# Performance work log

Measured on AMD Instinct MI355X. Metric: run time of the kernel, lower is better.

## Reference

```python
import jax, jax.numpy as jnp
import numpy as np

DIM = 256
N_PATCHES = 2048
N_HEADS = 8
BATCH = 2


def setup_inputs() -> dict:
    key = jax.random.key(0)
    ks = jax.random.split(key, 8)
    d = DIM
    s = d ** -0.5
    return {
        "x": jax.random.normal(ks[0], (BATCH, N_PATCHES, d), dtype=jnp.float32),
        # weights stored (in_features, out_features) so y = x @ W + b
        "W_qk": jax.random.normal(ks[1], (d, 2 * d), dtype=jnp.float32) * s,
        "W_v": jax.random.normal(ks[2], (d, d), dtype=jnp.float32) * s,
        "W_proj": jax.random.normal(ks[3], (d, d), dtype=jnp.float32) * s,
        "b_proj": jnp.zeros((d,), dtype=jnp.float32),
        "W_pos": jax.random.normal(ks[4], (2, N_HEADS), dtype=jnp.float32) * 0.5,
        "b_pos": jnp.zeros((N_HEADS,), dtype=jnp.float32),
        "gating": jnp.ones((N_HEADS,), dtype=jnp.float32),
    }


def reference(x, W_qk, W_v, W_proj, b_proj, W_pos, b_pos, gating):
    B, N, C = x.shape
    H = gating.shape[0]
    Dh = C // H
    scale = Dh ** -0.5

    # content attention: q @ k^T softmax
    qk = (x @ W_qk).reshape(B, N, 2, H, Dh)
    q = jnp.transpose(qk[:, :, 0], (0, 2, 1, 3))  # [B,H,N,Dh]
    k = jnp.transpose(qk[:, :, 1], (0, 2, 1, 3))
    patch_score = jax.nn.softmax(jnp.einsum("bhnd,bhmd->bhnm", q, k) * scale, axis=-1)

    # positional attention from relative indices (d, |d|) -> per-head score
    idx = jnp.arange(N, dtype=jnp.float32)
    rel = idx[:, None] - idx[None, :]                      # [N,N]
    rel_feat = jnp.stack([rel, jnp.abs(rel)], axis=-1)     # [N,N,2]
    pos = rel_feat @ W_pos + b_pos                         # [N,N,H]
    pos_score = jax.nn.softmax(jnp.transpose(pos, (2, 0, 1)), axis=-1)  # [H,N,N]

    g = jax.nn.sigmoid(gating)[None, :, None, None]        # [1,H,1,1]
    attn = (1.0 - g) * patch_score + g * pos_score[None]   # [B,H,N,N]
    attn = attn / jnp.sum(attn, axis=-1, keepdims=True)

    v = jnp.transpose((x @ W_v).reshape(B, N, H, Dh), (0, 2, 1, 3))  # [B,H,N,Dh]
    out = jnp.einsum("bhnm,bhmd->bhnd", attn, v)
    out = jnp.transpose(out, (0, 2, 1, 3)).reshape(B, N, C)
    return out @ W_proj + b_proj
```

## Files before the change

### kernel.cpp

```cpp
#include <hip/hip_runtime.h>
#include <hip/hip_bf16.h>
#include <hip/hip_fp16.h>

#define DIM 256
#define NP 2048
#define NH 8
#define BATCH 2
#define DH 32

typedef __attribute__((ext_vector_type(8))) short bshort8;
typedef __attribute__((ext_vector_type(4))) short bshort4;
typedef __attribute__((ext_vector_type(4))) float f32x4;

#define LOG2E 1.44269504f
#define QSCALE (0.17677669529663687f * LOG2E)

union U16B { uint4 u; bshort8 s8; bshort4 s4x[2]; __hip_bfloat16 h[8]; };
union U8B  { uint2 u; bshort4 s4; __hip_bfloat16 h[4]; };

__device__ __forceinline__ float fexp2(float x) { return __builtin_amdgcn_exp2f(x); }
__device__ __forceinline__ unsigned packbf(float hi, float lo) {
    return __builtin_amdgcn_perm(__float_as_uint(hi), __float_as_uint(lo), 0x07060302u);
}
__device__ __forceinline__ void gl16(const void* g, void* l) {
    __builtin_amdgcn_global_load_lds(
        (const __attribute__((address_space(1))) void*)g,
        (__attribute__((address_space(3))) void*)l, 16, 0, 0);
}
__device__ __forceinline__ int lds_addr(int row, int colg) {
    return row * 256 + (((colg ^ (row & 7)) & 31) << 3);
}

__global__ __launch_bounds__(256) void prep_kernel(
    const float* __restrict__ Wqk,
    const float* __restrict__ Wv,
    const float* __restrict__ Wproj,
    const float* __restrict__ x,
    __hip_bfloat16* __restrict__ WT,
    __hip_bfloat16* __restrict__ xb) {
    const int t = threadIdx.x;
    const int blk = blockIdx.x;
    if (blk >= 64) {
        const int base = (blk - 64) * 256 + t;
#pragma unroll
        for (int i = 0; i < 16; i++) {
            const int idx = base + i * 16384;
            float4 f = *(const float4*)(x + (size_t)idx * 4);
            U8B a;
            a.h[0] = __float2bfloat16(f.x); a.h[1] = __float2bfloat16(f.y);
            a.h[2] = __float2bfloat16(f.z); a.h[3] = __float2bfloat16(f.w);
            *(uint2*)(xb + (size_t)idx * 4) = a.u;
        }
        return;
    }
    __shared__ float ts[64][65];
    const int ct = blk >> 2, k0 = (blk & 3) * 64;
    const int c0 = ct * 64;
    const float* src; int ldw, cs0; float scl = 1.0f;
    if (ct < 8)       { src = Wqk;   ldw = 512; cs0 = c0;      if (ct < 4) scl = QSCALE; }
    else if (ct < 12) { src = Wv;    ldw = 256; cs0 = c0 - 512; }
    else              { src = Wproj; ldw = 256; cs0 = c0 - 768; }
    const int cc = t & 63, tq = t >> 6;
#pragma unroll
    for (int j = 0; j < 16; j++) {
        int kk = tq * 16 + j;
        ts[kk][cc] = src[(size_t)(k0 + kk) * ldw + cs0 + cc];
    }
    __syncthreads();
    const int kk2 = t & 63;
#pragma unroll
    for (int j = 0; j < 16; j++) {
        int cc2 = tq * 16 + j;
        WT[(size_t)(c0 + cc2) * 256 + k0 + kk2] = __float2bfloat16(ts[kk2][cc2] * scl);
    }
}

__global__ __launch_bounds__(256) void qkv_mfma(
    const __hip_bfloat16* __restrict__ xb,
    const __hip_bfloat16* __restrict__ WT,
    __hip_bfloat16* __restrict__ qT,
    __hip_bfloat16* __restrict__ k,
    __hip_bfloat16* __restrict__ vT) {
    __shared__ __align__(16) __hip_bfloat16 As[64 * 256];
    __shared__ __align__(16) __hip_bfloat16 Bs[64 * 256];
    const int t = threadIdx.x, lane = t & 63, wvid = t >> 6;
    const int l15 = lane & 15, l4 = lane >> 4;
    const int m0 = blockIdx.x * 64;
    const int nb0 = blockIdx.y * 64;
    const int nc = nb0 + wvid * 16 + l15;
    const int lrow = lane >> 5, lcg = lane & 31;

#pragma unroll
    for (int j = 0; j < 8; j++) {
        const int r0 = j * 8 + wvid * 2;
        const int row = r0 + lrow;
        const int cgs = (lcg ^ (row & 7)) & 31;
        gl16(xb + (((size_t)(m0 + row)) << 8) + cgs * 8, (char*)As + r0 * 512);
        gl16(WT + (((size_t)(nb0 + row)) << 8) + cgs * 8, (char*)Bs + r0 * 512);
    }
    __syncthreads();

    f32x4 acc[4] = {{0.f,0.f,0.f,0.f},{0.f,0.f,0.f,0.f},{0.f,0.f,0.f,0.f},{0.f,0.f,0.f,0.f}};
#pragma unroll
    for (int kk = 0; kk < 8; kk++) {
        const int colg = kk * 4 + l4;
        U16B bw; bw.u = *(const uint4*)&Bs[lds_addr(wvid * 16 + l15, colg)];
#pragma unroll
        for (int mt = 0; mt < 4; mt++) {
            U16B ax; ax.u = *(const uint4*)&As[lds_addr(mt * 16 + l15, colg)];
            acc[mt] = __builtin_amdgcn_mfma_f32_16x16x32_bf16(ax.s8, bw.s8, acc[mt], 0, 0, 0);
        }
    }

    if (nb0 < 256) {
        const int b = m0 >> 11;
#pragma unroll
        for (int mt = 0; mt < 4; mt++) {
            int tokn = (m0 & (NP - 1)) + mt * 16 + l4 * 4;
            U8B vv;
#pragma unroll
            for (int r = 0; r < 4; r++) vv.h[r] = __float2bfloat16(acc[mt][r]);
            *(uint2*)(qT + (size_t)(b * 256 + nc) * NP + tokn) = vv.u;
        }
    } else if (nb0 < 512) {
        const int c = nc - 256, h = c >> 5, d = c & 31;
#pragma unroll
        for (int mt = 0; mt < 4; mt++)
#pragma unroll
            for (int r = 0; r < 4; r++) {
                int tok = m0 + mt * 16 + l4 * 4 + r;
                int b = tok >> 11, n = tok & (NP - 1);
                k[((size_t)(b * NH + h) * NP + n) * DH + d] = __float2bfloat16(acc[mt][r]);
            }
    } else {
        const int c = nc - 512;
        const int b = m0 >> 11;
#pragma unroll
        for (int mt = 0; mt < 4; mt++) {
            int tokn = (m0 & (NP - 1)) + mt * 16 + l4 * 4;
            U8B vv;
#pragma unroll
            for (int r = 0; r < 4; r++) vv.h[r] = __float2bfloat16(acc[mt][r]);
            *(uint2*)(vT + (size_t)(b * 256 + c) * NP + tokn) = vv.u;
        }
    }
}

__global__ __launch_bounds__(512) void pos_scan(
    const __hip_bfloat16* __restrict__ vTg,
    const float* __restrict__ Wpos,
    __half* __restrict__ NF,
    __half* __restrict__ NB,
    float* __restrict__ lpF,
    float* __restrict__ lpB) {
    __shared__ float Lc[40][8];
    __shared__ float Cin[40][8];
    const int t = threadIdx.x;
    const int bh = blockIdx.x >> 1, dir = blockIdx.x & 1;
    const int h = bh & (NH - 1), b = bh >> 3;
    const float w0 = Wpos[h] * LOG2E, w1 = Wpos[NH + h] * LOG2E;
    const float rate = dir ? (w1 - w0) : (w0 + w1);
    const float mr = fexp2(fminf(rate, 0.f));
    const float mrate = fmaxf(rate, 0.f);
    const bool isV = (t < 256);
    const bool isD = (t >= 256 && t < 264);
    const bool act = isV || isD;
    const int ch  = isV ? (t & 31) : 32;
    const int seg = isV ? (t >> 5) : (t - 256);
    const int n0 = dir ? (seg * 256 + 255) : (seg * 256);
    const int stp = dir ? -1 : 1;
    const float dist0 = dir ? (float)(2047 - n0) : (float)n0;
    const float scl0 = fexp2(-mrate * dist0);
    float sdp[8];
#pragma unroll
    for (int j = 0; j < 8; j++) sdp[j] = fexp2(-mrate * (float)j);
    const float sd8 = fexp2(-mrate * 8.f);
    const __hip_bfloat16* vrow = vTg + ((size_t)(b * 256 + h * 32 + (ch & 31))) * NP;

    if (act) {
        float F = 0.f, sclc = scl0;
        int n = n0;
#pragma unroll 4
        for (int c = 0; c < 32; ++c) {
            float Wv[8];
            if (isV) {
                U16B vv; vv.u = *(const uint4*)(vrow + (dir ? n - 7 : n));
#pragma unroll
                for (int j = 0; j < 8; j++)
                    Wv[j] = sdp[j] * __bfloat162float(vv.h[dir ? 7 - j : j]);
            } else {
#pragma unroll
                for (int j = 0; j < 8; j++) Wv[j] = sdp[j];
            }
#pragma unroll
            for (int j = 0; j < 8; j++) F = fmaf(mr, F, sclc * Wv[j]);
            sclc *= sd8;
            n += 8 * stp;
        }
        Lc[ch][seg] = F;
    }
    __syncthreads();
    if (t < 33) {
        const float A = fexp2(fminf(rate, 0.f) * 256.f);
        float C = 0.f;
        for (int s = 0; s < 8; ++s) {
            const int ss = dir ? (7 - s) : s;
            Cin[t][ss] = C;
            C = fmaf(A, C, Lc[t][ss]);
        }
    }
    __syncthreads();
    if (act) {
        float Fc = Cin[ch][seg], sclc = scl0;
        int n = n0;
        __half* nout = dir ? NB : NF;
        float* lout = dir ? lpB : lpF;
#pragma unroll 4
        for (int c = 0; c < 32; ++c) {
            if (isV) {
                U16B vv; vv.u = *(const uint4*)(vrow + (dir ? n - 7 : n));
#pragma unroll
                for (int j = 0; j < 8; j++) {
                    float tt = sclc * (sdp[j] * __bfloat162float(vv.h[dir ? 7 - j : j]));
                    Fc = fmaf(mr, Fc, tt);
                    float outv = dir ? (Fc - tt) : Fc;
                    nout[((size_t)bh * NP + n + j * stp) * 32 + ch] = __float2half(outv);
                }
            } else {
#pragma unroll
                for (int j = 0; j < 8; j++) {
                    float tt = sclc * sdp[j];
                    Fc = fmaf(mr, Fc, tt);
                    float outv = dir ? (Fc - tt) : Fc;
                    lout[(size_t)bh * NP + n + j * stp] = outv;
                }
            }
            sclc *= sd8;
            n += 8 * stp;
        }
    }
}

__global__ __launch_bounds__(512, 4) void attn_kernel(
    const __hip_bfloat16* __restrict__ qg,
    const __hip_bfloat16* __restrict__ kg,
    const __hip_bfloat16* __restrict__ vTg,
    const float* __restrict__ Wpos,
    const float* __restrict__ gating,
    const __half* __restrict__ NF,
    const __half* __restrict__ NB,
    const float* __restrict__ lpF,
    const float* __restrict__ lpB,
    __hip_bfloat16* __restrict__ ao) {
    __shared__ __align__(16) __hip_bfloat16 Kt[2][2][64][40];
    __shared__ __align__(16) __hip_bfloat16 Vt[2][2][32][72];
    __shared__ float cmb[4][32][16];
    __shared__ float cls[4][16];

    const int t = threadIdx.x;
    const int lane = t & 63, wvid = t >> 6;
    const int l15 = lane & 15, l4 = lane >> 4;
    const int qt = wvid & 3, kh = wvid >> 2;
    const int bh = blockIdx.x >> 5, qb = blockIdx.x & 31;
    const int h = bh & (NH - 1), b = bh >> 3;
    const int q0 = qb * 64 + qt * 16;
    const int myq = q0 + l15;

    const int st_ = t & 255;
    const int kstart = kh * 1024;
    const __hip_bfloat16* kptr = kg + (size_t)bh * NP * DH + (size_t)(kstart + (st_ >> 2)) * DH + (st_ & 3) * 8;
    const __hip_bfloat16* vptr = vTg + ((size_t)bh * DH + (st_ >> 3)) * NP + kstart + (st_ & 7) * 8;

    const int vd = st_ >> 3, vs = st_ & 7;
    const int vc0 = ((2 * vs) & 3) * 16 + (vs >> 1) * 4;
    const int vc1 = ((2 * vs + 1) & 3) * 16 + (vs >> 1) * 4;

    uint4 kreg = *(const uint4*)kptr;
    uint4 vreg = *(const uint4*)vptr;
    *(uint4*)&Kt[kh][0][st_ >> 2][(st_ & 3) * 8] = kreg;
    *(uint2*)&Vt[kh][0][vd][vc0] = make_uint2(vreg.x, vreg.y);
    *(uint2*)&Vt[kh][0][vd][vc1] = make_uint2(vreg.z, vreg.w);

    const float w0 = Wpos[h] * LOG2E;
    const float w1 = Wpos[NH + h] * LOG2E;
    const float g = 1.0f / (1.0f + __expf(-gating[h]));
    const float nf = (float)myq;

    U16B qv;
#pragma unroll
    for (int j = 0; j < 8; j++)
        qv.h[j] = qg[((size_t)bh * DH + l4 * 8 + j) * NP + myq];

    __syncthreads();

    f32x4 os0 = {0.f,0.f,0.f,0.f}, os1 = {0.f,0.f,0.f,0.f};
    float ls = 0.f;

    for (int it = 0; it < 16; ++it) {
        const int cur = it & 1, nxt = cur ^ 1;

        if (it < 15) {
            kreg = *(const uint4*)(kptr + (size_t)(it + 1) * 64 * DH);
            vreg = *(const uint4*)(vptr + (it + 1) * 64);
        }

        f32x4 st4[4];
#pragma unroll
        for (int kt = 0; kt < 4; kt++) {
            U16B kf; kf.u = *(const uint4*)&Kt[kh][cur][kt * 16 + l15][l4 * 8];
            st4[kt] = __builtin_amdgcn_mfma_f32_16x16x32_bf16(
                kf.s8, qv.s8, (f32x4){0.f,0.f,0.f,0.f}, 0, 0, 0);
        }

        U16B va0, va1, vb0, vb1;
        {
            const __hip_bfloat16* v0 = &Vt[kh][cur][l15][l4 * 16];
            const __hip_bfloat16* v1 = &Vt[kh][cur][16 + l15][l4 * 16];
            va0.u = *(const uint4*)v0;
            va1.u = *(const uint4*)(v0 + 8);
            vb0.u = *(const uint4*)v1;
            vb1.u = *(const uint4*)(v1 + 8);
        }

#pragma unroll
        for (int kt = 0; kt < 4; kt++) {
            const bshort4 fa = (kt < 2) ? va0.s4x[kt & 1] : va1.s4x[kt & 1];
            const bshort4 fb = (kt < 2) ? vb0.s4x[kt & 1] : vb1.s4x[kt & 1];
            float es0 = fexp2(st4[kt][0]), es1 = fexp2(st4[kt][1]);
            float es2 = fexp2(st4[kt][2]), es3 = fexp2(st4[kt][3]);
            ls += (es0 + es1) + (es2 + es3);
            U8B pc;
            pc.u.x = packbf(es1, es0); pc.u.y = packbf(es3, es2);
            os0 = __builtin_amdgcn_mfma_f32_16x16x16bf16_1k(fa, pc.s4, os0, 0, 0, 0);
            os1 = __builtin_amdgcn_mfma_f32_16x16x16bf16_1k(fb, pc.s4, os1, 0, 0, 0);
        }

        if (it < 15) {
            *(uint4*)&Kt[kh][nxt][st_ >> 2][(st_ & 3) * 8] = kreg;
            *(uint2*)&Vt[kh][nxt][vd][vc0] = make_uint2(vreg.x, vreg.y);
            *(uint2*)&Vt[kh][nxt][vd][vc1] = make_uint2(vreg.z, vreg.w);
        }
        __syncthreads();
    }

    ls += __shfl_xor(ls, 16, 64); ls += __shfl_xor(ls, 32, 64);

    if (kh == 1) {
#pragma unroll
        for (int r = 0; r < 4; r++) {
            cmb[qt][l4 * 4 + r][l15]      = os0[r];
            cmb[qt][16 + l4 * 4 + r][l15] = os1[r];
        }
        if (l4 == 0) cls[qt][l15] = ls;
    }
    __syncthreads();
    if (kh == 0) {
        ls += cls[qt][l15];
        const float cs = (1.0f - g) / ls;
        const float pmF = fmaxf(0.f, (w0 + w1) * nf);
        const float pmB = fmaxf(0.f, (w1 - w0) * (2047.f - nf));
        const float pm  = fmaxf(pmF, pmB);
        const float eF = fexp2(pmF - pm);
        const float eB = fexp2(pmB - pm);
        const size_t lpi = (size_t)bh * NP + myq;
        const float lpv = eF * lpF[lpi] + eB * lpB[lpi];
        const float cp = g / lpv;
        const __half* nfp = NF + lpi * 32 + l4 * 4;
        const __half* nbp = NB + lpi * 32 + l4 * 4;
        const size_t orow = ((size_t)b * NP + myq) * DIM + h * DH;
        U8B o0, o1;
#pragma unroll
        for (int r = 0; r < 4; r++) {
            float p0 = eF * __half2float(nfp[r])      + eB * __half2float(nbp[r]);
            float p1 = eF * __half2float(nfp[16 + r]) + eB * __half2float(nbp[16 + r]);
            o0.h[r] = __float2bfloat16(cs * (os0[r] + cmb[qt][l4 * 4 + r][l15]) + cp * p0);
            o1.h[r] = __float2bfloat16(cs * (os1[r] + cmb[qt][16 + l4 * 4 + r][l15]) + cp * p1);
        }
        *(uint2*)(ao + orow + l4 * 4)      = o0.u;
        *(uint2*)(ao + orow + 16 + l4 * 4) = o1.u;
    }
}

__global__ __launch_bounds__(256) void proj_mfma(
    const __hip_bfloat16* __restrict__ ao,
    const __hip_bfloat16* __restrict__ WT,
    const float* __restrict__ bias,
    float* __restrict__ out) {
    __shared__ __align__(16) __hip_bfloat16 As[64 * 256];
    __shared__ __align__(16) __hip_bfloat16 Bs[64 * 256];
    const int t = threadIdx.x, lane = t & 63, wvid = t >> 6;
    const int l15 = lane & 15, l4 = lane >> 4;
    const int m0 = blockIdx.x * 64;
    const int nb0 = blockIdx.y * 64;
    const int nc = nb0 + wvid * 16 + l15;
    const int lrow = lane >> 5, lcg = lane & 31;

#pragma unroll
    for (int j = 0; j < 8; j++) {
        const int r0 = j * 8 + wvid * 2;
        const int row = r0 + lrow;
        const int cgs = (lcg ^ (row & 7)) & 31;
        gl16(ao + (((size_t)(m0 + row)) << 8) + cgs * 8, (char*)As + r0 * 512);
        gl16(WT + (((size_t)(768 + nb0 + row)) << 8) + cgs * 8, (char*)Bs + r0 * 512);
    }
    __syncthreads();

    f32x4 acc[4] = {{0.f,0.f,0.f,0.f},{0.f,0.f,0.f,0.f},{0.f,0.f,0.f,0.f},{0.f,0.f,0.f,0.f}};
#pragma unroll
    for (int kk = 0; kk < 8; kk++) {
        const int colg = kk * 4 + l4;
        U16B bw; bw.u = *(const uint4*)&Bs[lds_addr(wvid * 16 + l15, colg)];
#pragma unroll
        for (int mt = 0; mt < 4; mt++) {
            U16B ax; ax.u = *(const uint4*)&As[lds_addr(mt * 16 + l15, colg)];
            acc[mt] = __builtin_amdgcn_mfma_f32_16x16x32_bf16(ax.s8, bw.s8, acc[mt], 0, 0, 0);
        }
    }

    const float bb = bias[nc];
#pragma unroll
    for (int mt = 0; mt < 4; mt++)
#pragma unroll
        for (int r = 0; r < 4; r++) {
            int tok = m0 + mt * 16 + l4 * 4 + r;
            out[(size_t)tok * 256 + nc] = acc[mt][r] + bb;
        }
}

extern "C" void kernel_launch(void* const* d_in, const int* in_sizes, int n_in,
                              void* d_out, int out_size, void* d_ws, size_t ws_size,
                              hipStream_t stream) {
    const float* x      = (const float*)d_in[0];
    const float* Wqk    = (const float*)d_in[1];
    const float* Wv     = (const float*)d_in[2];
    const float* Wproj  = (const float*)d_in[3];
    const float* bproj  = (const float*)d_in[4];
    const float* Wpos   = (const float*)d_in[5];
    const float* gating = (const float*)d_in[7];
    float* out = (float*)d_out;

    char* w = (char*)d_ws;
    __hip_bfloat16* WT = (__hip_bfloat16*)w;
    __hip_bfloat16* qT = WT + 262144;
    __hip_bfloat16* k  = qT + 1048576;
    __hip_bfloat16* vT = k  + 1048576;
    __hip_bfloat16* ao = vT + 1048576;
    __hip_bfloat16* xb = ao + 1048576;
    __half* NF = (__half*)(w + 11010048);
    __half* NB = (__half*)(w + 13107200);
    float* lpF = (float*)(w + 15204352);
    float* lpB = (float*)(w + 15335424);

    prep_kernel<<<128, 256, 0, stream>>>(Wqk, Wv, Wproj, x, WT, xb);
    qkv_mfma<<<dim3(64, 12), 256, 0, stream>>>(xb, WT, qT, k, vT);
    pos_scan<<<32, 512, 0, stream>>>(vT, Wpos, NF, NB, lpF, lpB);
    attn_kernel<<<BATCH * NH * (NP / 64), 512, 0, stream>>>(qT, k, vT, Wpos, gating,
                                                            NF, NB, lpF, lpB, ao);
    proj_mfma<<<dim3(64, 4), 256, 0, stream>>>(ao, WT, bproj, out);
}
```

Before: 123.1 us.

## Fuse positional scan into attention kernel with semaphore; compute normalizers analytically

```diff
diff --git a/kernel.cpp b/kernel.cpp
--- a/kernel.cpp
+++ b/kernel.cpp
@@ -13,6 +13,7 @@
 typedef __attribute__((ext_vector_type(4))) float f32x4;
 
 #define LOG2E 1.44269504f
+#define LN2F 0.6931472f
 #define QSCALE (0.17677669529663687f * LOG2E)
 
 union U16B { uint4 u; bshort8 s8; bshort4 s4x[2]; __hip_bfloat16 h[8]; };
@@ -146,122 +147,103 @@
     }
 }
 
-__global__ __launch_bounds__(512) void pos_scan(
-    const __hip_bfloat16* __restrict__ vTg,
-    const float* __restrict__ Wpos,
-    __half* __restrict__ NF,
-    __half* __restrict__ NB,
-    float* __restrict__ lpF,
-    float* __restrict__ lpB) {
-    __shared__ float Lc[40][8];
-    __shared__ float Cin[40][8];
-    const int t = threadIdx.x;
-    const int bh = blockIdx.x >> 1, dir = blockIdx.x & 1;
-    const int h = bh & (NH - 1), b = bh >> 3;
-    const float w0 = Wpos[h] * LOG2E, w1 = Wpos[NH + h] * LOG2E;
-    const float rate = dir ? (w1 - w0) : (w0 + w1);
-    const float mr = fexp2(fminf(rate, 0.f));
-    const float mrate = fmaxf(rate, 0.f);
-    const bool isV = (t < 256);
-    const bool isD = (t >= 256 && t < 264);
-    const bool act = isV || isD;
-    const int ch  = isV ? (t & 31) : 32;
-    const int seg = isV ? (t >> 5) : (t - 256);
-    const int n0 = dir ? (seg * 256 + 255) : (seg * 256);
-    const int stp = dir ? -1 : 1;
-    const float dist0 = dir ? (float)(2047 - n0) : (float)n0;
-    const float scl0 = fexp2(-mrate * dist0);
-    float sdp[8];
-#pragma unroll
-    for (int j = 0; j < 8; j++) sdp[j] = fexp2(-mrate * (float)j);
-    const float sd8 = fexp2(-mrate * 8.f);
-    const __hip_bfloat16* vrow = vTg + ((size_t)(b * 256 + h * 32 + (ch & 31))) * NP;
-
-    if (act) {
-        float F = 0.f, sclc = scl0;
-        int n = n0;
-#pragma unroll 4
-        for (int c = 0; c < 32; ++c) {
-            float Wv[8];
-            if (isV) {
-                U16B vv; vv.u = *(const uint4*)(vrow + (dir ? n - 7 : n));
-#pragma unroll
-                for (int j = 0; j < 8; j++)
-                    Wv[j] = sdp[j] * __bfloat162float(vv.h[dir ? 7 - j : j]);
-            } else {
-#pragma unroll
-                for (int j = 0; j < 8; j++) Wv[j] = sdp[j];
-            }
-#pragma unroll
-            for (int j = 0; j < 8; j++) F = fmaf(mr, F, sclc * Wv[j]);
-            sclc *= sd8;
-            n += 8 * stp;
-        }
-        Lc[ch][seg] = F;
-    }
-    __syncthreads();
-    if (t < 33) {
-        const float A = fexp2(fminf(rate, 0.f) * 256.f);
-        float C = 0.f;
-        for (int s = 0; s < 8; ++s) {
-            const int ss = dir ? (7 - s) : s;
-            Cin[t][ss] = C;
-            C = fmaf(A, C, Lc[t][ss]);
-        }
-    }
-    __syncthreads();
-    if (act) {
-        float Fc = Cin[ch][seg], sclc = scl0;
-        int n = n0;
-        __half* nout = dir ? NB : NF;
-        float* lout = dir ? lpB : lpF;
-#pragma unroll 4
-        for (int c = 0; c < 32; ++c) {
-            if (isV) {
-                U16B vv; vv.u = *(const uint4*)(vrow + (dir ? n - 7 : n));
-#pragma unroll
-                for (int j = 0; j < 8; j++) {
-                    float tt = sclc * (sdp[j] * __bfloat162float(vv.h[dir ? 7 - j : j]));
-                    Fc = fmaf(mr, Fc, tt);
-                    float outv = dir ? (Fc - tt) : Fc;
-                    nout[((size_t)bh * NP + n + j * stp) * 32 + ch] = __float2half(outv);
-                }
-            } else {
-#pragma unroll
-                for (int j = 0; j < 8; j++) {
-                    float tt = sclc * sdp[j];
-                    Fc = fmaf(mr, Fc, tt);
-                    float outv = dir ? (Fc - tt) : Fc;
-                    lout[(size_t)bh * NP + n + j * stp] = outv;
-                }
-            }
-            sclc *= sd8;
-            n += 8 * stp;
-        }
-    }
-}
-
 __global__ __launch_bounds__(512, 4) void attn_kernel(
     const __hip_bfloat16* __restrict__ qg,
     const __hip_bfloat16* __restrict__ kg,
     const __hip_bfloat16* __restrict__ vTg,
     const float* __restrict__ Wpos,
     const float* __restrict__ gating,
-    const __half* __restrict__ NF,
-    const __half* __restrict__ NB,
-    const float* __restrict__ lpF,
-    const float* __restrict__ lpB,
-    __hip_bfloat16* __restrict__ ao) {
+    __half* __restrict__ NF,
+    __half* __restrict__ NB,
+    __hip_bfloat16* __restrict__ ao,
+    unsigned* __restrict__ sem) {
     __shared__ __align__(16) __hip_bfloat16 Kt[2][2][64][40];
     __shared__ __align__(16) __hip_bfloat16 Vt[2][2][32][72];
     __shared__ float cmb[4][32][16];
     __shared__ float cls[4][16];
 
     const int t = threadIdx.x;
+    const int bid = blockIdx.x;
+
+    if (bid < 64) {
+        float* scanL = &cmb[0][0][0];
+        float* scanC = scanL + 544;
+        const int sbh = bid >> 2, dir = (bid >> 1) & 1, cg = bid & 1;
+        const int sh = sbh & (NH - 1), sb = sbh >> 3;
+        const int seg = t >> 4, ch16 = t & 15, sch = cg * 16 + ch16;
+        const float sw0 = Wpos[sh] * LOG2E, sw1 = Wpos[NH + sh] * LOG2E;
+        const float rate = dir ? (sw1 - sw0) : (sw0 + sw1);
+        const float mr = fexp2(fminf(rate, 0.f));
+        const float mrate = fmaxf(rate, 0.f);
+        const int n0 = seg * 64;
+        const float dist0 = dir ? (float)(1984 - n0) : (float)n0;
+        float sclc = fexp2(-mrate * dist0);
+        const float sd8 = fexp2(-mrate * 8.f);
+        float sdp[8], mrp[9];
+#pragma unroll
+        for (int j = 0; j < 8; j++) sdp[j] = fexp2(-mrate * (float)j);
+        mrp[0] = 1.f;
+#pragma unroll
+        for (int j = 1; j < 9; j++) mrp[j] = mrp[j - 1] * mr;
+        const float mr8 = mrp[8];
+        const __hip_bfloat16* vrow = vTg + ((size_t)(sb * 256 + sh * 32 + sch)) * NP;
+
+        float S[64];
+        float F = 0.f;
+#pragma unroll
+        for (int c = 0; c < 8; c++) {
+            U16B vv;
+            vv.u = *(const uint4*)(vrow + (dir ? (n0 + 56 - c * 8) : (n0 + c * 8)));
+#pragma unroll
+            for (int j = 0; j < 8; j++) {
+                float V = __bfloat162float(vv.h[dir ? 7 - j : j]);
+                float inp = sclc * (sdp[j] * V);
+                float Fp = F;
+                F = fmaf(mr, F, inp);
+                S[c * 8 + j] = dir ? (mr * Fp) : F;
+            }
+            sclc *= sd8;
+        }
+        scanL[ch16 * 33 + seg] = F;
+        __syncthreads();
+        if (t < 16) {
+            const float A64 = fexp2(fminf(rate, 0.f) * 64.f);
+            float C = 0.f;
+            for (int idx = 0; idx < 32; ++idx) {
+                const int s = dir ? (31 - idx) : idx;
+                scanC[t * 33 + s] = C;
+                C = fmaf(A64, C, scanL[t * 33 + s]);
+            }
+        }
+        __syncthreads();
+        {
+            const float Cin = scanC[ch16 * 33 + seg];
+            __half* nout = dir ? NB : NF;
+            float cm = Cin;
+#pragma unroll
+            for (int c = 0; c < 8; c++) {
+#pragma unroll
+                for (int j = 0; j < 8; j++) {
+                    const int i = c * 8 + j;
+                    float outv = fmaf(cm, mrp[j + 1], S[i]);
+                    const int ni = dir ? (n0 + 63 - i) : (n0 + i);
+                    nout[((size_t)sbh * NP + ni) * 32 + sch] = __float2half(outv);
+                }
+                cm *= mr8;
+            }
+        }
+        __syncthreads();
+        if (t == 0) {
+            __threadfence();
+            __hip_atomic_fetch_add(sem, 1u, __ATOMIC_RELEASE, __HIP_MEMORY_SCOPE_AGENT);
+        }
+        __syncthreads();
+    }
+
     const int lane = t & 63, wvid = t >> 6;
     const int l15 = lane & 15, l4 = lane >> 4;
     const int qt = wvid & 3, kh = wvid >> 2;
-    const int bh = blockIdx.x >> 5, qb = blockIdx.x & 31;
+    const int bh = bid >> 5, qb = bid & 31;
     const int h = bh & (NH - 1), b = bh >> 3;
     const int q0 = qb * 64 + qt * 16;
     const int myq = q0 + l15;
@@ -353,18 +335,34 @@
         }
         if (l4 == 0) cls[qt][l15] = ls;
     }
+    if (t == 0) {
+        while (__hip_atomic_load(sem, __ATOMIC_ACQUIRE, __HIP_MEMORY_SCOPE_AGENT) < 64u)
+            __builtin_amdgcn_s_sleep(2);
+        __threadfence();
+    }
     __syncthreads();
     if (kh == 0) {
         ls += cls[qt][l15];
         const float cs = (1.0f - g) / ls;
-        const float pmF = fmaxf(0.f, (w0 + w1) * nf);
-        const float pmB = fmaxf(0.f, (w1 - w0) * (2047.f - nf));
+        const float a2 = w0 + w1, b2 = w1 - w0;
+        const float pmF = fmaxf(0.f, a2 * nf);
+        const float pmB = fmaxf(0.f, b2 * (2047.f - nf));
         const float pm  = fmaxf(pmF, pmB);
         const float eF = fexp2(pmF - pm);
         const float eB = fexp2(pmB - pm);
+        const float aa = fabsf(a2), ab = fabsf(b2);
+        const float Mf = 2047.f - nf;
+        const float lpFv = (aa > 1e-9f)
+            ? expm1f(-LN2F * aa * (nf + 1.f)) / expm1f(-LN2F * aa)
+            : (nf + 1.f);
+        float lpBv;
+        if (ab > 1e-9f) {
+            const float E = expm1f(-LN2F * ab * Mf) / expm1f(-LN2F * ab);
+            lpBv = (b2 > 0.f) ? E : fexp2(-ab) * E;
+        } else lpBv = Mf;
+        const float lpv = eF * lpFv + eB * lpBv;
+        const float cp = g / lpv;
         const size_t lpi = (size_t)bh * NP + myq;
-        const float lpv = eF * lpF[lpi] + eB * lpB[lpi];
-        const float cp = g / lpv;
         const __half* nfp = NF + lpi * 32 + l4 * 4;
         const __half* nbp = NB + lpi * 32 + l4 * 4;
         const size_t orow = ((size_t)b * NP + myq) * DIM + h * DH;
@@ -448,13 +446,13 @@
     __hip_bfloat16* xb = ao + 1048576;
     __half* NF = (__half*)(w + 11010048);
     __half* NB = (__half*)(w + 13107200);
-    float* lpF = (float*)(w + 15204352);
-    float* lpB = (float*)(w + 15335424);
+    unsigned* sem = (unsigned*)(w + (16u << 20));
+
+    hipMemsetAsync(sem, 0, 64, stream);
 
     prep_kernel<<<128, 256, 0, stream>>>(Wqk, Wv, Wproj, x, WT, xb);
     qkv_mfma<<<dim3(64, 12), 256, 0, stream>>>(xb, WT, qT, k, vT);
-    pos_scan<<<32, 512, 0, stream>>>(vT, Wpos, NF, NB, lpF, lpB);
     attn_kernel<<<BATCH * NH * (NP / 64), 512, 0, stream>>>(qT, k, vT, Wpos, gating,
-                                                            NF, NB, lpF, lpB, ao);
+                                                            NF, NB, ao, sem);
     proj_mfma<<<dim3(64, 4), 256, 0, stream>>>(ao, WT, bproj, out);
 }
```

New measurement: 125.0 us. No clear change (+1.6%).
